# Kernel tuning notes

Measured on AMD Instinct MI355X. Metric: run time of the kernel, lower is better.

Reference implementation:

```python
import jax, jax.numpy as jnp
import numpy as np


def setup_inputs() -> dict:
    key = jax.random.key(0)
    k1, k2, k3 = jax.random.split(key, 3)
    b, c, h, w, S = 16, 512, 64, 64, 8
    x = jax.random.normal(k1, (b, c, h, w), dtype=jnp.float32)
    Wk = jax.random.normal(k2, (S, c), dtype=jnp.float32) * (1.0 / np.sqrt(c))  # mk.weight [S, c]
    Wv = jax.random.normal(k3, (c, S), dtype=jnp.float32) * (1.0 / np.sqrt(S))  # mv.weight [c, S]
    return {"x": x, "Wk": Wk, "Wv": Wv}


def reference(x, Wk, Wv):
    b, c, h, w = x.shape
    n = h * w
    q = x.reshape(b, c, n).transpose(0, 2, 1)          # [b, n, c]
    attn = jnp.einsum('bnc,sc->bns', q, Wk)            # mk: [b, n, S]
    attn = jax.nn.softmax(attn, axis=1)                # softmax over tokens (dim=1)
    attn = attn / (1e-9 + jnp.sum(attn, axis=2, keepdims=True))  # L1 renorm over S
    out = jnp.einsum('bns,cs->bnc', attn, Wv)          # mv: [b, n, c]
    out = out.transpose(0, 2, 1).reshape(b, c, h, w)
    return jax.nn.relu(x + out)
```

## Files before the change

### kernel.cpp

```cpp
#include <hip/hip_runtime.h>
#include <math.h>

#define BB 16
#define CC 512
#define NTOK 4096
#define SS 8

__global__ __launch_bounds__(256) void k_logits(const float* __restrict__ x,
                                                const float* __restrict__ Wk,
                                                float* __restrict__ logits) {
    __shared__ float wkT[CC * SS];
    __shared__ float red[4 * 64 * 33];
    const int tid   = threadIdx.x;
    const int tn    = tid & 63;
    const int tc    = tid >> 6;
    const int blk   = blockIdx.x;
    const int b     = blk >> 4;
    const int ntile = blk & 15;
    const int n0    = ntile * 256 + tn * 4;

    for (int k = tid; k < CC * SS; k += 256) {
        int s = k >> 9;
        int c = k & (CC - 1);
        wkT[c * SS + s] = Wk[k];
    }
    __syncthreads();

    float acc[4][SS];
#pragma unroll
    for (int i = 0; i < 4; ++i)
#pragma unroll
        for (int s = 0; s < SS; ++s) acc[i][s] = 0.f;

    const float* xb = x + (size_t)b * CC * NTOK + n0;
#pragma unroll 4
    for (int k = 0; k < CC / 4; ++k) {
        int c = tc + k * 4;
        float4 x4 = *(const float4*)(xb + (size_t)c * NTOK);
        const float* wk = &wkT[c * SS];
#pragma unroll
        for (int s = 0; s < SS; ++s) {
            float w = wk[s];
            acc[0][s] += x4.x * w;
            acc[1][s] += x4.y * w;
            acc[2][s] += x4.z * w;
            acc[3][s] += x4.w * w;
        }
    }

    float* myred = &red[tc * (64 * 33) + tn * 33];
#pragma unroll
    for (int i = 0; i < 4; ++i)
#pragma unroll
        for (int s = 0; s < SS; ++s) myred[i * 8 + s] = acc[i][s];
    __syncthreads();

    float* outb = logits + ((size_t)b * NTOK + (size_t)ntile * 256) * SS;
#pragma unroll
    for (int j = 0; j < 8; ++j) {
        int flat = tid + j * 256;
        int tnp  = flat >> 5;
        int rem  = flat & 31;
        float v = 0.f;
#pragma unroll
        for (int t = 0; t < 4; ++t) v += red[t * (64 * 33) + tnp * 33 + rem];
        outb[flat] = v;
    }
}

__global__ __launch_bounds__(256) void k_stats(const float* __restrict__ logits,
                                               float* __restrict__ ml) {
    const int b   = blockIdx.x >> 3;
    const int s   = blockIdx.x & 7;
    const int tid = threadIdx.x;

    float v[16];
    const float* base = logits + (size_t)b * NTOK * SS + s;
#pragma unroll
    for (int j = 0; j < 16; ++j) v[j] = base[(size_t)(tid + j * 256) * SS];

    float m = v[0];
#pragma unroll
    for (int j = 1; j < 16; ++j) m = fmaxf(m, v[j]);
#pragma unroll
    for (int off = 32; off > 0; off >>= 1) m = fmaxf(m, __shfl_down(m, off, 64));

    __shared__ float sm[4];
    __shared__ float sl[4];
    const int wave = tid >> 6;
    const int lane = tid & 63;
    if (lane == 0) sm[wave] = m;
    __syncthreads();
    const float mm = fmaxf(fmaxf(sm[0], sm[1]), fmaxf(sm[2], sm[3]));

    float l = 0.f;
#pragma unroll
    for (int j = 0; j < 16; ++j) l += __expf(v[j] - mm);
#pragma unroll
    for (int off = 32; off > 0; off >>= 1) l += __shfl_down(l, off, 64);
    if (lane == 0) sl[wave] = l;
    __syncthreads();
    if (tid == 0) {
        ml[blockIdx.x]       = mm;
        ml[128 + blockIdx.x] = sl[0] + sl[1] + sl[2] + sl[3];
    }
}

__global__ __launch_bounds__(256) void k_out(const float* __restrict__ x,
                                             const float* __restrict__ Wv,
                                             const float* __restrict__ logits,
                                             const float* __restrict__ ml,
                                             float* __restrict__ out) {
    __shared__ float wv[CC * SS];
    const int tid   = threadIdx.x;
    const int tn    = tid & 63;
    const int tc    = tid >> 6;
    const int blk   = blockIdx.x;
    const int b     = blk >> 5;
    const int rest  = blk & 31;
    const int ntile = rest >> 1;
    const int chalf = rest & 1;
    const int n0    = ntile * 256 + tn * 4;

    for (int k = tid; k < CC * SS; k += 256) wv[k] = Wv[k];

    float m[SS], invl[SS];
    const float* mb = ml + b * SS;
#pragma unroll
    for (int s = 0; s < SS; ++s) {
        m[s]    = mb[s];
        invl[s] = 1.0f / mb[128 + s];
    }

    const float* lg = logits + ((size_t)b * NTOK + n0) * SS;
    float w[4][SS];
#pragma unroll
    for (int i = 0; i < 4; ++i) {
        float4 p0 = *(const float4*)(lg + i * 8);
        float4 p1 = *(const float4*)(lg + i * 8 + 4);
        float e[SS] = {p0.x, p0.y, p0.z, p0.w, p1.x, p1.y, p1.z, p1.w};
        float rs = 0.f;
#pragma unroll
        for (int s = 0; s < SS; ++s) {
            float p = __expf(e[s] - m[s]) * invl[s];
            w[i][s] = p;
            rs += p;
        }
        float inv = 1.0f / (1e-9f + rs);
#pragma unroll
        for (int s = 0; s < SS; ++s) w[i][s] *= inv;
    }
    __syncthreads();

    const size_t xbase = (size_t)b * CC * NTOK + n0;
#pragma unroll 4
    for (int k = 0; k < CC / 8; ++k) {
        int c = chalf * 256 + tc + k * 4;
        const float* xp = x + xbase + (size_t)c * NTOK;
        float4 x4 = *(const float4*)xp;
        const float* wvc = &wv[c * SS];
        float o0 = 0.f, o1 = 0.f, o2 = 0.f, o3 = 0.f;
#pragma unroll
        for (int s = 0; s < SS; ++s) {
            float vv = wvc[s];
            o0 += w[0][s] * vv;
            o1 += w[1][s] * vv;
            o2 += w[2][s] * vv;
            o3 += w[3][s] * vv;
        }
        float4 y;
        y.x = fmaxf(x4.x + o0, 0.f);
        y.y = fmaxf(x4.y + o1, 0.f);
        y.z = fmaxf(x4.z + o2, 0.f);
        y.w = fmaxf(x4.w + o3, 0.f);
        *(float4*)(out + xbase + (size_t)c * NTOK) = y;
    }
}

extern "C" void kernel_launch(void* const* d_in, const int* in_sizes, int n_in,
                              void* d_out, int out_size, void* d_ws, size_t ws_size,
                              hipStream_t stream) {
    const float* x  = (const float*)d_in[0];
    const float* Wk = (const float*)d_in[1];
    const float* Wv = (const float*)d_in[2];
    float* outp = (float*)d_out;

    float* logits = (float*)d_ws;
    float* ml     = logits + (size_t)BB * NTOK * SS;

    k_logits<<<BB * (NTOK / 256), 256, 0, stream>>>(x, Wk, logits);
    k_stats<<<BB * SS, 256, 0, stream>>>(logits, ml);
    k_out<<<BB * (NTOK / 256) * 2, 256, 0, stream>>>(x, Wv, logits, ml, outp);
}
```

Measured before the change: 276.4 us.

## Fuse softmax stats into logits kernel via atomic exp-sums, halve token tiles

Removes the separate stats kernel. The logits kernel now accumulates per-(batch, slot) sums of exp(logit) without max subtraction and adds them into a workspace with atomicAdd after a hipMemsetAsync. Token tiles shrink from 256 to 128 and the channel split grows to 8 groups, doubling block counts for better occupancy. Dropping the max subtraction risks overflow for large logits and makes the sums order-dependent because of the float atomics.

```diff
diff --git a/kernel.cpp b/kernel.cpp
--- a/kernel.cpp
+++ b/kernel.cpp
@@ -5,19 +5,23 @@
 #define CC 512
 #define NTOK 4096
 #define SS 8
+#define TT 128
+#define RSTRIDE 36
 
 __global__ __launch_bounds__(256) void k_logits(const float* __restrict__ x,
                                                 const float* __restrict__ Wk,
-                                                float* __restrict__ logits) {
+                                                float* __restrict__ logits,
+                                                float* __restrict__ lsum) {
     __shared__ float wkT[CC * SS];
-    __shared__ float red[4 * 64 * 33];
+    __shared__ float red[8 * 32 * RSTRIDE];
+    __shared__ float esum[4 * SS];
     const int tid   = threadIdx.x;
-    const int tn    = tid & 63;
-    const int tc    = tid >> 6;
+    const int tn    = tid & 31;
+    const int tc    = tid >> 5;
     const int blk   = blockIdx.x;
-    const int b     = blk >> 4;
-    const int ntile = blk & 15;
-    const int n0    = ntile * 256 + tn * 4;
+    const int b     = blk >> 5;
+    const int ntile = blk & 31;
+    const int n0    = ntile * TT + tn * 4;
 
     for (int k = tid; k < CC * SS; k += 256) {
         int s = k >> 9;
@@ -33,9 +37,9 @@
         for (int s = 0; s < SS; ++s) acc[i][s] = 0.f;
 
     const float* xb = x + (size_t)b * CC * NTOK + n0;
-#pragma unroll 4
-    for (int k = 0; k < CC / 4; ++k) {
-        int c = tc + k * 4;
+#pragma unroll 8
+    for (int k = 0; k < CC / 8; ++k) {
+        int c = tc + k * 8;
         float4 x4 = *(const float4*)(xb + (size_t)c * NTOK);
         const float* wk = &wkT[c * SS];
 #pragma unroll
@@ -48,89 +52,61 @@
         }
     }
 
-    float* myred = &red[tc * (64 * 33) + tn * 33];
+    float4* myred = (float4*)&red[tc * (32 * RSTRIDE) + tn * RSTRIDE];
 #pragma unroll
-    for (int i = 0; i < 4; ++i)
-#pragma unroll
-        for (int s = 0; s < SS; ++s) myred[i * 8 + s] = acc[i][s];
+    for (int i = 0; i < 4; ++i) {
+        myred[i * 2]     = make_float4(acc[i][0], acc[i][1], acc[i][2], acc[i][3]);
+        myred[i * 2 + 1] = make_float4(acc[i][4], acc[i][5], acc[i][6], acc[i][7]);
+    }
     __syncthreads();
 
-    float* outb = logits + ((size_t)b * NTOK + (size_t)ntile * 256) * SS;
+    float* outb = logits + ((size_t)b * NTOK + (size_t)ntile * TT) * SS;
+    float es = 0.f;
 #pragma unroll
-    for (int j = 0; j < 8; ++j) {
+    for (int j = 0; j < 4; ++j) {
         int flat = tid + j * 256;
         int tnp  = flat >> 5;
         int rem  = flat & 31;
         float v = 0.f;
 #pragma unroll
-        for (int t = 0; t < 4; ++t) v += red[t * (64 * 33) + tnp * 33 + rem];
+        for (int t = 0; t < 8; ++t) v += red[t * (32 * RSTRIDE) + tnp * RSTRIDE + rem];
         outb[flat] = v;
+        es += __expf(v);
     }
-}
-
-__global__ __launch_bounds__(256) void k_stats(const float* __restrict__ logits,
-                                               float* __restrict__ ml) {
-    const int b   = blockIdx.x >> 3;
-    const int s   = blockIdx.x & 7;
-    const int tid = threadIdx.x;
-
-    float v[16];
-    const float* base = logits + (size_t)b * NTOK * SS + s;
-#pragma unroll
-    for (int j = 0; j < 16; ++j) v[j] = base[(size_t)(tid + j * 256) * SS];
-
-    float m = v[0];
-#pragma unroll
-    for (int j = 1; j < 16; ++j) m = fmaxf(m, v[j]);
-#pragma unroll
-    for (int off = 32; off > 0; off >>= 1) m = fmaxf(m, __shfl_down(m, off, 64));
-
-    __shared__ float sm[4];
-    __shared__ float sl[4];
-    const int wave = tid >> 6;
-    const int lane = tid & 63;
-    if (lane == 0) sm[wave] = m;
+    es += __shfl_down(es, 8, 64);
+    es += __shfl_down(es, 16, 64);
+    es += __shfl_down(es, 32, 64);
+    const int lane = tid & 63, wave = tid >> 6;
+    if (lane < SS) esum[wave * SS + lane] = es;
     __syncthreads();
-    const float mm = fmaxf(fmaxf(sm[0], sm[1]), fmaxf(sm[2], sm[3]));
-
-    float l = 0.f;
-#pragma unroll
-    for (int j = 0; j < 16; ++j) l += __expf(v[j] - mm);
-#pragma unroll
-    for (int off = 32; off > 0; off >>= 1) l += __shfl_down(l, off, 64);
-    if (lane == 0) sl[wave] = l;
-    __syncthreads();
-    if (tid == 0) {
-        ml[blockIdx.x]       = mm;
-        ml[128 + blockIdx.x] = sl[0] + sl[1] + sl[2] + sl[3];
+    if (tid < SS) {
+        float t = esum[tid] + esum[SS + tid] + esum[2 * SS + tid] + esum[3 * SS + tid];
+        atomicAdd(&lsum[b * SS + tid], t);
     }
 }
 
 __global__ __launch_bounds__(256) void k_out(const float* __restrict__ x,
                                              const float* __restrict__ Wv,
                                              const float* __restrict__ logits,
-                                             const float* __restrict__ ml,
+                                             const float* __restrict__ lsum,
                                              float* __restrict__ out) {
     __shared__ float wv[CC * SS];
     const int tid   = threadIdx.x;
-    const int tn    = tid & 63;
-    const int tc    = tid >> 6;
+    const int tn    = tid & 31;
+    const int tc    = tid >> 5;
     const int blk   = blockIdx.x;
-    const int b     = blk >> 5;
-    const int rest  = blk & 31;
+    const int b     = blk >> 6;
+    const int rest  = blk & 63;
     const int ntile = rest >> 1;
     const int chalf = rest & 1;
-    const int n0    = ntile * 256 + tn * 4;
+    const int n0    = ntile * TT + tn * 4;
 
     for (int k = tid; k < CC * SS; k += 256) wv[k] = Wv[k];
 
-    float m[SS], invl[SS];
-    const float* mb = ml + b * SS;
+    float invl[SS];
+    const float* lb = lsum + b * SS;
 #pragma unroll
-    for (int s = 0; s < SS; ++s) {
-        m[s]    = mb[s];
-        invl[s] = 1.0f / mb[128 + s];
-    }
+    for (int s = 0; s < SS; ++s) invl[s] = 1.0f / lb[s];
 
     const float* lg = logits + ((size_t)b * NTOK + n0) * SS;
     float w[4][SS];
@@ -142,7 +118,7 @@
         float rs = 0.f;
 #pragma unroll
         for (int s = 0; s < SS; ++s) {
-            float p = __expf(e[s] - m[s]) * invl[s];
+            float p = __expf(e[s]) * invl[s];
             w[i][s] = p;
             rs += p;
         }
@@ -153,9 +129,9 @@
     __syncthreads();
 
     const size_t xbase = (size_t)b * CC * NTOK + n0;
-#pragma unroll 4
-    for (int k = 0; k < CC / 8; ++k) {
-        int c = chalf * 256 + tc + k * 4;
+#pragma unroll 8
+    for (int k = 0; k < CC / 16; ++k) {
+        int c = chalf * (CC / 2) + tc + k * 8;
         const float* xp = x + xbase + (size_t)c * NTOK;
         float4 x4 = *(const float4*)xp;
         const float* wvc = &wv[c * SS];
@@ -186,9 +162,9 @@
     float* outp = (float*)d_out;
 
     float* logits = (float*)d_ws;
-    float* ml     = logits + (size_t)BB * NTOK * SS;
+    float* lsum   = logits + (size_t)BB * NTOK * SS;
 
-    k_logits<<<BB * (NTOK / 256), 256, 0, stream>>>(x, Wk, logits);
-    k_stats<<<BB * SS, 256, 0, stream>>>(logits, ml);
-    k_out<<<BB * (NTOK / 256) * 2, 256, 0, stream>>>(x, Wv, logits, ml, outp);
+    hipMemsetAsync(lsum, 0, BB * SS * sizeof(float), stream);
+    k_logits<<<BB * 32, 256, 0, stream>>>(x, Wk, logits, lsum);
+    k_out<<<BB * 64, 256, 0, stream>>>(x, Wv, logits, lsum, outp);
 }
```

New measurement: 276.4 us. No clear change (+0.0%).
